# Optimization experiments

Measured on AMD Instinct MI355X. Metric: run time of the kernel, lower is better.

## Reference

```python
import jax, jax.numpy as jnp
import numpy as np
from jax.ops import segment_sum, segment_max

N = 20000      # nodes
DEG = 16       # incoming edges per node
E = N * DEG    # edges
IN = 128       # in_features
BOND = 16      # bond_features_dim
OUT = 128      # output_features
NUM_LAYERS = 3
LEAKY = 0.2
ELU_ALPHA = 1.0


def _lin_params(key, out_f, in_f):
    kw, kb = jax.random.split(key)
    s = 1.0 / np.sqrt(in_f)
    w = jax.random.uniform(kw, (out_f, in_f), jnp.float32, -s, s)
    b = jax.random.uniform(kb, (out_f,), jnp.float32, -s, s)
    return w, b


def setup_inputs() -> dict:
    key = jax.random.key(0)
    ks = jax.random.split(key, 20)
    atom_features = jax.random.normal(ks[0], (N, IN), jnp.float32)
    edge_src = jax.random.randint(ks[1], (E,), 0, N, jnp.int32)
    # every node receives exactly DEG edges (avoids the isolated-node bug path)
    edge_dst = jnp.repeat(jnp.arange(N, dtype=jnp.int32), DEG)
    bond_features = jax.random.normal(ks[2], (E, BOND), jnp.float32)

    v1_fc1_w, v1_fc1_b = _lin_params(ks[3], OUT, IN)
    v1_fc2_w, v1_fc2_b = _lin_params(ks[4], OUT, IN + BOND)
    v1_att_w, v1_att_b = _lin_params(ks[5], 1, 2 * OUT)
    v1_attend_w, v1_attend_b = _lin_params(ks[6], OUT, OUT)
    v1_gru_wih, v1_gru_bih = _lin_params(ks[7], 3 * OUT, OUT)
    v1_gru_whh, v1_gru_bhh = _lin_params(ks[8], 3 * OUT, OUT)

    v2_fc1_w, v2_fc1_b = _lin_params(ks[9], 1, 2 * OUT)
    v2_fc2_w, v2_fc2_b = _lin_params(ks[10], OUT, OUT)
    v2_gru_wih, v2_gru_bih = _lin_params(ks[11], 3 * OUT, OUT)
    v2_gru_whh, v2_gru_bhh = _lin_params(ks[12], 3 * OUT, OUT)

    lin_w, lin_b = _lin_params(ks[13], OUT, OUT)

    return dict(atom_features=atom_features, edge_src=edge_src, edge_dst=edge_dst,
                bond_features=bond_features,
                v1_fc1_w=v1_fc1_w, v1_fc1_b=v1_fc1_b, v1_fc2_w=v1_fc2_w, v1_fc2_b=v1_fc2_b,
                v1_att_w=v1_att_w, v1_att_b=v1_att_b, v1_attend_w=v1_attend_w, v1_attend_b=v1_attend_b,
                v1_gru_wih=v1_gru_wih, v1_gru_whh=v1_gru_whh, v1_gru_bih=v1_gru_bih, v1_gru_bhh=v1_gru_bhh,
                v2_fc1_w=v2_fc1_w, v2_fc1_b=v2_fc1_b, v2_fc2_w=v2_fc2_w, v2_fc2_b=v2_fc2_b,
                v2_gru_wih=v2_gru_wih, v2_gru_whh=v2_gru_whh, v2_gru_bih=v2_gru_bih, v2_gru_bhh=v2_gru_bhh,
                lin_w=lin_w, lin_b=lin_b)


def _linear(x, w, b):
    return x @ w.T + b


def _gru_cell(x, h, wih, whh, bih, bhh):
    gi = x @ wih.T + bih   # [N, 3*OUT]
    gh = h @ whh.T + bhh
    i_r, i_z, i_n = jnp.split(gi, 3, axis=-1)
    h_r, h_z, h_n = jnp.split(gh, 3, axis=-1)
    r = jax.nn.sigmoid(i_r + h_r)
    z = jax.nn.sigmoid(i_z + h_z)
    n = jnp.tanh(i_n + r * h_n)
    return (1.0 - z) * n + z * h


def _segment_softmax(logits, seg, n):
    m = segment_max(logits, seg, num_segments=n)
    ex = jnp.exp(logits - m[seg])
    den = segment_sum(ex, seg, num_segments=n)
    return ex / den[seg]


def reference(atom_features, edge_src, edge_dst, bond_features,
              v1_fc1_w, v1_fc1_b, v1_fc2_w, v1_fc2_b, v1_att_w, v1_att_b,
              v1_attend_w, v1_attend_b, v1_gru_wih, v1_gru_whh, v1_gru_bih, v1_gru_bhh,
              v2_fc1_w, v2_fc1_b, v2_fc2_w, v2_fc2_b,
              v2_gru_wih, v2_gru_whh, v2_gru_bih, v2_gru_bhh,
              lin_w, lin_b):
    n = atom_features.shape[0]
    lrelu = lambda x: jax.nn.leaky_relu(x, negative_slope=LEAKY)

    # ---- GATlayerV1 ----
    new_atom = lrelu(_linear(atom_features, v1_fc1_w, v1_fc1_b))           # [N, OUT]
    nbr_trans = _linear(new_atom, v1_attend_w, v1_attend_b)                # [N, OUT]
    nbr_in = jnp.concatenate([atom_features[edge_src], bond_features], axis=1)  # [E, IN+BOND]
    nbr = lrelu(_linear(nbr_in, v1_fc2_w, v1_fc2_b))                       # [E, OUT]
    pair = jnp.concatenate([new_atom[edge_dst], nbr], axis=1)              # [E, 2*OUT]
    logits = lrelu(_linear(pair, v1_att_w, v1_att_b))[:, 0]                # [E]
    score = _segment_softmax(logits, edge_dst, n)                          # [E]
    transform = segment_sum(score[:, None] * nbr_trans[edge_src], edge_dst, num_segments=n)
    ctx = jax.nn.elu(transform, alpha=ELU_ALPHA)
    h = _gru_cell(ctx, new_atom, v1_gru_wih, v1_gru_whh, v1_gru_bih, v1_gru_bhh)
    G_0 = new_atom

    all_tensors = [h]

    # ---- GATlayerV2 (shared weights across layers 2..NUM_LAYERS) ----
    for _ in range(NUM_LAYERS - 1):
        nt = _linear(h, v2_fc2_w, v2_fc2_b)                                # [N, OUT]
        pair2 = jnp.concatenate([h[edge_dst], h[edge_src]], axis=1)        # [E, 2*OUT]
        lg = lrelu(_linear(pair2, v2_fc1_w, v2_fc1_b))[:, 0]               # [E]
        sc = _segment_softmax(lg, edge_dst, n)
        tr = segment_sum(sc[:, None] * nt[edge_src], edge_dst, num_segments=n)
        ctx2 = jax.nn.elu(tr, alpha=ELU_ALPHA)
        h = _gru_cell(ctx2, h, v2_gru_wih, v2_gru_whh, v2_gru_bih, v2_gru_bhh)
        all_tensors.append(h)

    all_stack = jnp.stack(all_tensors)           # [NUM_LAYERS, N, OUT]
    averaged = all_stack.mean(axis=0)            # [N, OUT]
    output = jax.nn.gelu(_linear(averaged, lin_w, lin_b), approximate=False)
    return (output, all_stack, G_0, averaged)
```

## Files before the change

kernel.cpp:

```cpp
#include <hip/hip_runtime.h>
#include <math.h>

#define NN 20000
#define EE 320000

using short8 = __attribute__((ext_vector_type(8))) short;
using f32x4  = __attribute__((ext_vector_type(4))) float;
using f32x2  = __attribute__((ext_vector_type(2))) float;
using u16x4  = __attribute__((ext_vector_type(4))) unsigned short;

__device__ __forceinline__ unsigned short f2bf(float x) {
    union { float f; unsigned u; } v; v.f = x;
    unsigned r = (v.u + 0x7fffu + ((v.u >> 16) & 1u)) >> 16;
    return (unsigned short)r;
}
__device__ __forceinline__ float bf2f(unsigned short b) {
    union { unsigned u; float f; } v; v.u = ((unsigned)b) << 16;
    return v.f;
}
__device__ __forceinline__ float sigmoidf_(float x) { return 1.f / (1.f + __expf(-x)); }
__device__ __forceinline__ float tanhf_(float x) {
    float e = __expf(-2.f * x);
    return (1.f - e) / (1.f + e);
}
__device__ __forceinline__ float lrelu_(float x) { return x > 0.f ? x : 0.2f * x; }
__device__ __forceinline__ float elu_(float x) { return x > 0.f ? x : __expf(x) - 1.f; }

__device__ __forceinline__ unsigned pk_fp8x4(float a, float b, float c, float d) {
    int w = 0;
    w = __builtin_amdgcn_cvt_pk_fp8_f32(a, b, w, false);
    w = __builtin_amdgcn_cvt_pk_fp8_f32(c, d, w, true);
    return (unsigned)w;
}
__device__ __forceinline__ void up_fp8x4(unsigned w, float* o) {
    f32x2 lo = __builtin_amdgcn_cvt_pk_f32_fp8((int)w, false);
    f32x2 hi = __builtin_amdgcn_cvt_pk_f32_fp8((int)w, true);
    o[0] = lo[0]; o[1] = lo[1]; o[2] = hi[0]; o[3] = hi[1];
}

struct PackDesc { const float* w; unsigned short* out; int O; int ldw; int mode; };
struct PackArgs { PackDesc d[10]; };

__global__ void k_pack(PackArgs args) {
    PackDesc d = args.d[blockIdx.y];
    int idx = blockIdx.x * 256 + threadIdx.x;
    if (d.mode == 1) {
        if (idx >= 512) return;
        int t = idx >> 6, l = idx & 63;
        int lr = l & 15, lg = l >> 4;
        int ch = lr * 8 + t;
        short8 o;
        #pragma unroll
        for (int j = 0; j < 8; j++) {
            int k = lg * 8 + j;
            o[j] = (k < 16) ? (short)f2bf(d.w[(size_t)ch * 144 + 128 + k]) : (short)0;
        }
        *(short8*)(d.out + (size_t)idx * 8) = o;
        return;
    }
    int total = (d.O / 16) * 4 * 64;
    if (idx >= total) return;
    int l = idx & 63, rest = idx >> 6;
    int ko = rest & 3, no = rest >> 2;
    int row = no * 16 + (l & 15);
    int col0 = ko * 32 + ((l >> 4) * 8);
    const float* src = d.w + (size_t)row * d.ldw + col0;
    unsigned short o[8];
    #pragma unroll
    for (int j = 0; j < 8; j++) o[j] = f2bf(src[j]);
    #pragma unroll
    for (int j = 0; j < 8; j++) d.out[(size_t)idx * 8 + j] = o[j];
}

__global__ __launch_bounds__(256) void k_v1_front(
    const float* __restrict__ atom,
    const unsigned short* __restrict__ Bfc1, const unsigned short* __restrict__ BW2a,
    const float* __restrict__ fc1_b, const float* __restrict__ fc2_b,
    const float* __restrict__ attw,
    float* __restrict__ g0, unsigned short* __restrict__ naBf,
    unsigned char* __restrict__ naF8,
    unsigned char* __restrict__ U8, float* __restrict__ adst)
{
    __shared__ float Xs[16][132];
    __shared__ unsigned short Ys2[16 * 128];
    const int tid = threadIdx.x, l = tid & 63, w = tid >> 6;
    const int lr = l & 15, lg = l >> 4;
    const int m0 = blockIdx.x * 16;

    f32x4 acc1[2] = {}, accU[2] = {};
    #pragma unroll
    for (int ko = 0; ko < 4; ko++) {
        const f32x4* ap = (const f32x4*)(atom + (size_t)(m0 + lr) * 128 + ko * 32 + lg * 8);
        f32x4 a0 = __builtin_nontemporal_load(ap);
        f32x4 a1 = __builtin_nontemporal_load(ap + 1);
        short8 af;
        #pragma unroll
        for (int j = 0; j < 4; j++) { af[j] = (short)f2bf(a0[j]); af[4 + j] = (short)f2bf(a1[j]); }
        #pragma unroll
        for (int i = 0; i < 2; i++) {
            int t = w * 2 + i;
            short8 b1 = *(const short8*)(Bfc1 + ((size_t)(t * 4 + ko) * 64 + l) * 8);
            acc1[i] = __builtin_amdgcn_mfma_f32_16x16x32_bf16(af, b1, acc1[i], 0, 0, 0);
            short8 bu = *(const short8*)(BW2a + ((size_t)(t * 4 + ko) * 64 + l) * 8);
            accU[i] = __builtin_amdgcn_mfma_f32_16x16x32_bf16(af, bu, accU[i], 0, 0, 0);
        }
    }
    #pragma unroll
    for (int i = 0; i < 2; i++) {
        int col = (w * 2 + i) * 16 + lr;
        float b1v = fc1_b[col], bUv = fc2_b[col];
        #pragma unroll
        for (int r = 0; r < 4; r++) {
            int row = lg * 4 + r;
            float v = lrelu_(acc1[i][r] + b1v);
            Xs[row][col] = v;
            Ys2[row * 128 + col] = f2bf(accU[i][r] + bUv);
        }
    }
    __syncthreads();
    {
        short8 uy = *(const short8*)(Ys2 + tid * 8);
        float uf[8];
        #pragma unroll
        for (int j = 0; j < 8; j++) uf[j] = bf2f((unsigned short)uy[j]);
        uint2 o8;
        o8.x = pk_fp8x4(uf[0], uf[1], uf[2], uf[3]);
        o8.y = pk_fp8x4(uf[4], uf[5], uf[6], uf[7]);
        *(uint2*)(U8 + (size_t)m0 * 128 + tid * 8) = o8;
    }
    {
        int row = tid >> 4, q = tid & 15;
        short8 tmp;
        float p = 0.f;
        float vv[8];
        #pragma unroll
        for (int j = 0; j < 8; j++) {
            float x = Xs[row][q * 8 + j];
            vv[j] = x;
            tmp[j] = (short)f2bf(x);
            p = fmaf(x, attw[q * 8 + j], p);
        }
        __builtin_nontemporal_store(*(f32x4*)vv,
            (f32x4*)(g0 + (size_t)(m0 + row) * 128 + q * 8));
        __builtin_nontemporal_store(*(f32x4*)(vv + 4),
            (f32x4*)(g0 + (size_t)(m0 + row) * 128 + q * 8 + 4));
        *(short8*)(naBf + (size_t)(m0 + row) * 128 + q * 8) = tmp;
        uint2 n8;
        n8.x = pk_fp8x4(vv[0], vv[1], vv[2], vv[3]);
        n8.y = pk_fp8x4(vv[4], vv[5], vv[6], vv[7]);
        *(uint2*)(naF8 + (size_t)(m0 + row) * 128 + q * 8) = n8;
        #pragma unroll
        for (int m = 1; m <= 8; m <<= 1) p += __shfl_xor(p, m, 16);
        if (q == 0) adst[m0 + row] = p;
    }
}

template<int AGGMODE, int FRONT, int FINAL>
__global__ __launch_bounds__(512, 4) void k_gru(
    const float* __restrict__ aD, const float* __restrict__ bS, const float* __restrict__ b1,
    const float* __restrict__ bond, const unsigned short* __restrict__ BW2b,
    const float* __restrict__ attw, const float* __restrict__ attb1,
    const float* __restrict__ adst, const unsigned char* __restrict__ U8,
    const int* __restrict__ esrc, const unsigned char* __restrict__ V8,
    const unsigned short* __restrict__ Bpre, const float* __restrict__ bpre,
    const unsigned short* __restrict__ Bih, const unsigned short* __restrict__ Bhh,
    const float* __restrict__ bih, const float* __restrict__ bhh,
    const unsigned short* __restrict__ hprevBf, float* __restrict__ houtF,
    unsigned short* __restrict__ houtBf, unsigned char* __restrict__ houtF8,
    const float* __restrict__ w2att, float* __restrict__ aDOut, float* __restrict__ bSOut,
    const float* __restrict__ as0, const float* __restrict__ as1,
    const unsigned short* __restrict__ Blin, const float* __restrict__ linb,
    float* __restrict__ avgOut, float* __restrict__ outF)
{
    __shared__ unsigned short aggS[16][136];
    __shared__ unsigned short ctxS[16][136];
    __shared__ unsigned short hpS[16][136];
    __shared__ float lgS[(AGGMODE == 0) ? 16 : 1][16];
    const int tid = threadIdx.x, l = tid & 63, w = tid >> 6;
    const int lr = l & 15, lg = l >> 4;
    const int m0 = blockIdx.x * 16;
    const int r2 = tid >> 5, c4 = (tid & 31) * 4;

    *(u16x4*)&hpS[r2][c4] = *(const u16x4*)(hprevBf + (size_t)(m0 + r2) * 128 + c4);

    if (AGGMODE == 0) {
        float aw[8];
        #pragma unroll
        for (int t = 0; t < 8; t++) aw[t] = attw[128 + lr * 8 + t];
        const float ab = attb1[0];
        #pragma unroll
        for (int nn = 0; nn < 2; nn++) {
            const int n = m0 + w * 2 + nn;
            const int e0 = n * 16;
            short8 af = {};
            if (lg < 2) {
                const f32x4* bp = (const f32x4*)(bond + (size_t)(e0 + lr) * 16 + lg * 8);
                f32x4 b0 = __builtin_nontemporal_load(bp);
                f32x4 b1v = __builtin_nontemporal_load(bp + 1);
                #pragma unroll
                for (int j = 0; j < 4; j++) {
                    af[j] = (short)f2bf(b0[j]); af[4 + j] = (short)f2bf(b1v[j]);
                }
            }
            f32x4 c[8];
            #pragma unroll
            for (int t = 0; t < 8; t++) {
                short8 bw = *(const short8*)(BW2b + (size_t)(t * 64 + l) * 8);
                f32x4 z = {};
                c[t] = __builtin_amdgcn_mfma_f32_16x16x32_bf16(af, bw, z, 0, 0, 0);
            }
            float s[4];
            #pragma unroll
            for (int r = 0; r < 4; r++) {
                int e = e0 + lg * 4 + r;
                int src = esrc[e];
                uint2 u2 = *(const uint2*)(U8 + (size_t)src * 128 + lr * 8);
                float uf[8];
                up_fp8x4(u2.x, uf);
                up_fp8x4(u2.y, uf + 4);
                float a0 = 0.f;
                #pragma unroll
                for (int t = 0; t < 8; t++)
                    a0 = fmaf(aw[t], lrelu_(c[t][r] + uf[t]), a0);
                s[r] = a0;
            }
            #pragma unroll
            for (int mk = 1; mk <= 8; mk <<= 1)
                #pragma unroll
                for (int r = 0; r < 4; r++) s[r] += __shfl_xor(s[r], mk, 16);
            if (lr == 0) {
                float anode = adst[n];
                #pragma unroll
                for (int r = 0; r < 4; r++)
                    lgS[w * 2 + nn][lg * 4 + r] = lrelu_(anode + ab + s[r]);
            }
        }
    }
    __syncthreads();

    const int g2 = tid >> 5;
    const int q2 = tid & 31;
    const int q = q2 & 15;
    const int hf = q2 >> 4;
    float wq;
    int srcq;
    {
        const int gnode = m0 + g2;
        const int e = gnode * 16 + q;
        srcq = esrc[e];
        float lgt;
        if (AGGMODE == 0) lgt = lgS[g2][q];
        else              lgt = lrelu_(aD[gnode] + bS[srcq] + b1[0]);
        float mx = lgt;
        #pragma unroll
        for (int mk = 1; mk <= 8; mk <<= 1) mx = fmaxf(mx, __shfl_xor(mx, mk, 16));
        float ex = __expf(lgt - mx);
        float den = ex;
        #pragma unroll
        for (int mk = 1; mk <= 8; mk <<= 1) den += __shfl_xor(den, mk, 16);
        wq = ex / den;
    }

    unsigned gv[16];
    #pragma unroll
    for (int i = 0; i < 16; i++) {
        int si = __shfl(srcq, i, 16);
        gv[i] = *(const unsigned*)(V8 + (size_t)si * 128 + hf * 64 + q * 4);
    }

    f32x4 ah[3] = {};
    #pragma unroll
    for (int ko = 0; ko < 4; ko++) {
        short8 afh = *(const short8*)&hpS[lr][ko * 32 + lg * 8];
        #pragma unroll
        for (int g = 0; g < 3; g++) {
            short8 bh = *(const short8*)(Bhh + ((size_t)((w + 8 * g) * 4 + ko) * 64 + l) * 8);
            ah[g] = __builtin_amdgcn_mfma_f32_16x16x32_bf16(afh, bh, ah[g], 0, 0, 0);
        }
    }

    {
        float s[4] = {};
        #pragma unroll
        for (int i = 0; i < 16; i++) {
            float wi = __shfl(wq, i, 16);
            float d[4];
            up_fp8x4(gv[i], d);
            #pragma unroll
            for (int j = 0; j < 4; j++) s[j] = fmaf(wi, d[j], s[j]);
        }
        u16x4 o;
        #pragma unroll
        for (int j = 0; j < 4; j++) o[j] = f2bf(s[j]);
        *(u16x4*)&aggS[g2][hf * 64 + q * 4] = o;
    }
    __syncthreads();

    f32x4 accp = {};
    #pragma unroll
    for (int ko = 0; ko < 4; ko++) {
        short8 afA = *(const short8*)&aggS[lr][ko * 32 + lg * 8];
        short8 bfp = *(const short8*)(Bpre + ((size_t)(w * 4 + ko) * 64 + l) * 8);
        accp = __builtin_amdgcn_mfma_f32_16x16x32_bf16(afA, bfp, accp, 0, 0, 0);
    }
    {
        const int col = w * 16 + lr;
        const float bb = bpre[col];
        #pragma unroll
        for (int r = 0; r < 4; r++)
            ctxS[lg * 4 + r][col] = f2bf(elu_(accp[r] + bb));
    }
    __syncthreads();

    f32x4 ai[3] = {};
    #pragma unroll
    for (int ko = 0; ko < 4; ko++) {
        short8 afc = *(const short8*)&ctxS[lr][ko * 32 + lg * 8];
        #pragma unroll
        for (int g = 0; g < 3; g++) {
            short8 bi = *(const short8*)(Bih + ((size_t)((w + 8 * g) * 4 + ko) * 64 + l) * 8);
            ai[g] = __builtin_amdgcn_mfma_f32_16x16x32_bf16(afc, bi, ai[g], 0, 0, 0);
        }
    }
    {
        const int c = w * 16 + lr;
        const float br = bih[c] + bhh[c];
        const float bz = bih[c + 128] + bhh[c + 128];
        const float bin_ = bih[c + 256];
        const float bhn = bhh[c + 256];
        #pragma unroll
        for (int r = 0; r < 4; r++) {
            const int lrow = lg * 4 + r;
            float rg = sigmoidf_(ai[0][r] + ah[0][r] + br);
            float zg = sigmoidf_(ai[1][r] + ah[1][r] + bz);
            float ng = tanhf_(ai[2][r] + bin_ + rg * (ah[2][r] + bhn));
            float hp = bf2f(hpS[lrow][c]);
            hpS[lrow][c] = f2bf(fmaf(zg, hp - ng, ng));
        }
    }
    __syncthreads();

    {
        u16x4 hv = *(const u16x4*)&hpS[r2][c4];
        f32x4 vf;
        #pragma unroll
        for (int j = 0; j < 4; j++) vf[j] = bf2f(hv[j]);
        __builtin_nontemporal_store(vf, (f32x4*)(houtF + (size_t)(m0 + r2) * 128 + c4));
        if (FINAL == 0) {
            *(u16x4*)(houtBf + (size_t)(m0 + r2) * 128 + c4) = hv;
            *(unsigned*)(houtF8 + (size_t)(m0 + r2) * 128 + c4) =
                pk_fp8x4(vf[0], vf[1], vf[2], vf[3]);
        }
    }

    if (FRONT) {
        if (tid < 256) {
            int row = tid >> 4, qq = tid & 15;
            short8 hv8 = *(const short8*)&hpS[row][qq * 8];
            float pa = 0.f, pb = 0.f;
            #pragma unroll
            for (int j = 0; j < 8; j++) {
                float x = bf2f((unsigned short)hv8[j]);
                pa = fmaf(x, w2att[qq * 8 + j], pa);
                pb = fmaf(x, w2att[128 + qq * 8 + j], pb);
            }
            #pragma unroll
            for (int m = 1; m <= 8; m <<= 1) {
                pa += __shfl_xor(pa, m, 16);
                pb += __shfl_xor(pb, m, 16);
            }
            if (qq == 0) { aDOut[m0 + row] = pa; bSOut[m0 + row] = pb; }
        }
    }

    if (FINAL) {
        {
            f32x4 x0 = __builtin_nontemporal_load(
                (const f32x4*)(as0 + (size_t)(m0 + r2) * 128 + c4));
            f32x4 x1 = __builtin_nontemporal_load(
                (const f32x4*)(as1 + (size_t)(m0 + r2) * 128 + c4));
            u16x4 hv = *(const u16x4*)&hpS[r2][c4];
            f32x4 av;
            #pragma unroll
            for (int j = 0; j < 4; j++)
                av[j] = (x0[j] + x1[j] + bf2f(hv[j])) * (1.f / 3.f);
            __builtin_nontemporal_store(av, (f32x4*)(avgOut + (size_t)(m0 + r2) * 128 + c4));
            u16x4 ab16;
            #pragma unroll
            for (int j = 0; j < 4; j++) ab16[j] = f2bf(av[j]);
            *(u16x4*)&ctxS[r2][c4] = ab16;
        }
        __syncthreads();
        f32x4 acc2 = {};
        #pragma unroll
        for (int ko = 0; ko < 4; ko++) {
            short8 af = *(const short8*)&ctxS[lr][ko * 32 + lg * 8];
            short8 bf = *(const short8*)(Blin + ((size_t)(w * 4 + ko) * 64 + l) * 8);
            acc2 = __builtin_amdgcn_mfma_f32_16x16x32_bf16(af, bf, acc2, 0, 0, 0);
        }
        {
            const int col = w * 16 + lr;
            const float bb = linb[col];
            #pragma unroll
            for (int r = 0; r < 4; r++) {
                float vv = acc2[r] + bb;
                vv = 0.5f * vv * (1.f + erff(vv * 0.70710678118654752f));
                aggS[lg * 4 + r][col] = f2bf(vv);
            }
        }
        __syncthreads();
        {
            u16x4 ov = *(const u16x4*)&aggS[r2][c4];
            f32x4 vf;
            #pragma unroll
            for (int j = 0; j < 4; j++) vf[j] = bf2f(ov[j]);
            __builtin_nontemporal_store(vf, (f32x4*)(outF + (size_t)(m0 + r2) * 128 + c4));
        }
    }
}

extern "C" void kernel_launch(void* const* d_in, const int* in_sizes, int n_in,
                              void* d_out, int out_size, void* d_ws, size_t ws_size,
                              hipStream_t stream) {
    const float* atom     = (const float*)d_in[0];
    const int*   esrc     = (const int*)d_in[1];
    const float* bond     = (const float*)d_in[3];
    const float* fc1_w    = (const float*)d_in[4];
    const float* fc1_b    = (const float*)d_in[5];
    const float* fc2_w    = (const float*)d_in[6];
    const float* fc2_b    = (const float*)d_in[7];
    const float* att_w    = (const float*)d_in[8];
    const float* att_b    = (const float*)d_in[9];
    const float* attend_w = (const float*)d_in[10];
    const float* attend_b = (const float*)d_in[11];
    const float* gih1     = (const float*)d_in[12];
    const float* ghh1     = (const float*)d_in[13];
    const float* bih1     = (const float*)d_in[14];
    const float* bhh1     = (const float*)d_in[15];
    const float* fc1v2_w  = (const float*)d_in[16];
    const float* fc1v2_b  = (const float*)d_in[17];
    const float* fc2v2_w  = (const float*)d_in[18];
    const float* fc2v2_b  = (const float*)d_in[19];
    const float* gih2     = (const float*)d_in[20];
    const float* ghh2     = (const float*)d_in[21];
    const float* bih2     = (const float*)d_in[22];
    const float* bhh2     = (const float*)d_in[23];
    const float* lin_w    = (const float*)d_in[24];
    const float* lin_b    = (const float*)d_in[25];

    char* wsb = (char*)d_ws;
    size_t off = 0;
    auto allocB = [&](size_t bytes) {
        size_t o = off; off = (off + bytes + 255) & ~(size_t)255; return o;
    };
    unsigned short* Bfc1   = (unsigned short*)(wsb + allocB(128 * 128 * 2));
    unsigned short* Batt   = (unsigned short*)(wsb + allocB(128 * 128 * 2));
    unsigned short* BW2a   = (unsigned short*)(wsb + allocB(128 * 128 * 2));
    unsigned short* BW2b   = (unsigned short*)(wsb + allocB(512 * 8 * 2));
    unsigned short* Bgih1  = (unsigned short*)(wsb + allocB(384 * 128 * 2));
    unsigned short* Bghh1  = (unsigned short*)(wsb + allocB(384 * 128 * 2));
    unsigned short* Bfc2v2 = (unsigned short*)(wsb + allocB(128 * 128 * 2));
    unsigned short* Bgih2  = (unsigned short*)(wsb + allocB(384 * 128 * 2));
    unsigned short* Bghh2  = (unsigned short*)(wsb + allocB(384 * 128 * 2));
    unsigned short* Blin   = (unsigned short*)(wsb + allocB(128 * 128 * 2));
    unsigned short* naBf   = (unsigned short*)(wsb + allocB((size_t)NN * 128 * 2));
    unsigned short* h1Bf   = (unsigned short*)(wsb + allocB((size_t)NN * 128 * 2));
    unsigned short* h2Bf   = (unsigned short*)(wsb + allocB((size_t)NN * 128 * 2));
    unsigned char*  U8     = (unsigned char*)(wsb + allocB((size_t)NN * 128));
    unsigned char*  naF8   = (unsigned char*)(wsb + allocB((size_t)NN * 128));
    unsigned char*  h1F8   = (unsigned char*)(wsb + allocB((size_t)NN * 128));
    unsigned char*  h2F8   = (unsigned char*)(wsb + allocB((size_t)NN * 128));
    float* adst   = (float*)(wsb + allocB((size_t)NN * 4));
    float* aD     = (float*)(wsb + allocB((size_t)NN * 4));
    float* bS     = (float*)(wsb + allocB((size_t)NN * 4));
    (void)ws_size;

    float* out0 = (float*)d_out;
    float* as0  = out0 + (size_t)NN * 128;
    float* as1  = as0 + (size_t)NN * 128;
    float* as2  = as1 + (size_t)NN * 128;
    float* g0   = out0 + (size_t)4 * NN * 128;
    float* avg  = out0 + (size_t)5 * NN * 128;

    PackArgs pa;
    pa.d[0] = { fc1_w,    Bfc1,   128, 128, 0 };
    pa.d[1] = { attend_w, Batt,   128, 128, 0 };
    pa.d[2] = { fc2_w,    BW2a,   128, 144, 0 };
    pa.d[3] = { gih1,     Bgih1,  384, 128, 0 };
    pa.d[4] = { ghh1,     Bghh1,  384, 128, 0 };
    pa.d[5] = { fc2v2_w,  Bfc2v2, 128, 128, 0 };
    pa.d[6] = { gih2,     Bgih2,  384, 128, 0 };
    pa.d[7] = { ghh2,     Bghh2,  384, 128, 0 };
    pa.d[8] = { lin_w,    Blin,   128, 128, 0 };
    pa.d[9] = { fc2_w,    BW2b,   0,   0,   1 };
    k_pack<<<dim3(24, 10), 256, 0, stream>>>(pa);

    const int GB = NN / 16;

    k_v1_front<<<GB, 256, 0, stream>>>(atom, Bfc1, BW2a, fc1_b, fc2_b, att_w,
                                       g0, naBf, naF8, U8, adst);
    k_gru<0, 1, 0><<<GB, 512, 0, stream>>>(
        nullptr, nullptr, nullptr,
        bond, BW2b, att_w, att_b, adst, U8,
        esrc, naF8,
        Batt, attend_b,
        Bgih1, Bghh1, bih1, bhh1, naBf, as0, h1Bf, h1F8,
        fc1v2_w, aD, bS,
        nullptr, nullptr, nullptr, nullptr, nullptr, nullptr);

    k_gru<1, 1, 0><<<GB, 512, 0, stream>>>(
        aD, bS, fc1v2_b,
        nullptr, nullptr, nullptr, nullptr, nullptr, nullptr,
        esrc, h1F8,
        Bfc2v2, fc2v2_b,
        Bgih2, Bghh2, bih2, bhh2, h1Bf, as1, h2Bf, h2F8,
        fc1v2_w, aD, bS,
        nullptr, nullptr, nullptr, nullptr, nullptr, nullptr);

    k_gru<1, 0, 1><<<GB, 512, 0, stream>>>(
        aD, bS, fc1v2_b,
        nullptr, nullptr, nullptr, nullptr, nullptr, nullptr,
        esrc, h2F8,
        Bfc2v2, fc2v2_b,
        Bgih2, Bghh2, bih2, bhh2, h2Bf, as2, nullptr, nullptr,
        nullptr, nullptr, nullptr,
        as0, as1, Blin, lin_b, avg, out0);
}
```

Measured before the change: 113.6 us.

## Halve k_gru block to 256 threads, two column tiles per wave

Shrinks the fused GRU/attention kernel from 512 to 256 threads per 16-node block, so each of the 4 waves now computes two 16-column MFMA tiles per gate and each thread handles 8 features in the gather and store phases. Work per thread doubles, which raises register pressure but cuts the number of waves taking part in each barrier and amortizes A-fragment LDS loads across two B tiles. With fewer waves per block, latency hiding relies on more concurrent blocks per CU, and occupancy could drop if registers grow.

```diff
diff --git a/kernel.cpp b/kernel.cpp
--- a/kernel.cpp
+++ b/kernel.cpp
@@ -156,7 +156,7 @@
 }
 
 template<int AGGMODE, int FRONT, int FINAL>
-__global__ __launch_bounds__(512, 4) void k_gru(
+__global__ __launch_bounds__(256, 4) void k_gru(
     const float* __restrict__ aD, const float* __restrict__ bS, const float* __restrict__ b1,
     const float* __restrict__ bond, const unsigned short* __restrict__ BW2b,
     const float* __restrict__ attw, const float* __restrict__ attb1,
@@ -179,9 +179,9 @@
     const int tid = threadIdx.x, l = tid & 63, w = tid >> 6;
     const int lr = l & 15, lg = l >> 4;
     const int m0 = blockIdx.x * 16;
-    const int r2 = tid >> 5, c4 = (tid & 31) * 4;
-
-    *(u16x4*)&hpS[r2][c4] = *(const u16x4*)(hprevBf + (size_t)(m0 + r2) * 128 + c4);
+    const int r2 = tid >> 4, sc0 = (tid & 15) * 8;
+
+    *(short8*)&hpS[r2][sc0] = *(const short8*)(hprevBf + (size_t)(m0 + r2) * 128 + sc0);
 
     if (AGGMODE == 0) {
         float aw[8];
@@ -189,8 +189,8 @@
         for (int t = 0; t < 8; t++) aw[t] = attw[128 + lr * 8 + t];
         const float ab = attb1[0];
         #pragma unroll
-        for (int nn = 0; nn < 2; nn++) {
-            const int n = m0 + w * 2 + nn;
+        for (int nn = 0; nn < 4; nn++) {
+            const int n = m0 + w * 4 + nn;
             const int e0 = n * 16;
             short8 af = {};
             if (lg < 2) {
@@ -232,22 +232,19 @@
                 float anode = adst[n];
                 #pragma unroll
                 for (int r = 0; r < 4; r++)
-                    lgS[w * 2 + nn][lg * 4 + r] = lrelu_(anode + ab + s[r]);
+                    lgS[w * 4 + nn][lg * 4 + r] = lrelu_(anode + ab + s[r]);
             }
         }
     }
     __syncthreads();
 
-    const int g2 = tid >> 5;
-    const int q2 = tid & 31;
-    const int q = q2 & 15;
-    const int hf = q2 >> 4;
+    const int g2 = tid >> 4;
+    const int q = tid & 15;
     float wq;
     int srcq;
     {
         const int gnode = m0 + g2;
-        const int e = gnode * 16 + q;
-        srcq = esrc[e];
+        srcq = esrc[gnode * 16 + q];
         float lgt;
         if (AGGMODE == 0) lgt = lgS[g2][q];
         else              lgt = lrelu_(aD[gnode] + bS[srcq] + b1[0]);
@@ -261,69 +258,81 @@
         wq = ex / den;
     }
 
-    unsigned gv[16];
+    uint2 gv[16];
     #pragma unroll
     for (int i = 0; i < 16; i++) {
         int si = __shfl(srcq, i, 16);
-        gv[i] = *(const unsigned*)(V8 + (size_t)si * 128 + hf * 64 + q * 4);
-    }
-
-    f32x4 ah[3] = {};
+        gv[i] = *(const uint2*)(V8 + (size_t)si * 128 + q * 8);
+    }
+
+    f32x4 ah[2][3] = {};
     #pragma unroll
     for (int ko = 0; ko < 4; ko++) {
         short8 afh = *(const short8*)&hpS[lr][ko * 32 + lg * 8];
         #pragma unroll
-        for (int g = 0; g < 3; g++) {
-            short8 bh = *(const short8*)(Bhh + ((size_t)((w + 8 * g) * 4 + ko) * 64 + l) * 8);
-            ah[g] = __builtin_amdgcn_mfma_f32_16x16x32_bf16(afh, bh, ah[g], 0, 0, 0);
-        }
+        for (int g = 0; g < 3; g++)
+            #pragma unroll
+            for (int ct = 0; ct < 2; ct++) {
+                int t = w + ct * 4 + 8 * g;
+                short8 bh = *(const short8*)(Bhh + ((size_t)(t * 4 + ko) * 64 + l) * 8);
+                ah[ct][g] = __builtin_amdgcn_mfma_f32_16x16x32_bf16(afh, bh, ah[ct][g], 0, 0, 0);
+            }
     }
 
     {
-        float s[4] = {};
+        float s[8] = {};
         #pragma unroll
         for (int i = 0; i < 16; i++) {
             float wi = __shfl(wq, i, 16);
-            float d[4];
-            up_fp8x4(gv[i], d);
-            #pragma unroll
-            for (int j = 0; j < 4; j++) s[j] = fmaf(wi, d[j], s[j]);
-        }
-        u16x4 o;
-        #pragma unroll
-        for (int j = 0; j < 4; j++) o[j] = f2bf(s[j]);
-        *(u16x4*)&aggS[g2][hf * 64 + q * 4] = o;
+            float d[8];
+            up_fp8x4(gv[i].x, d);
+            up_fp8x4(gv[i].y, d + 4);
+            #pragma unroll
+            for (int j = 0; j < 8; j++) s[j] = fmaf(wi, d[j], s[j]);
+        }
+        short8 o;
+        #pragma unroll
+        for (int j = 0; j < 8; j++) o[j] = (short)f2bf(s[j]);
+        *(short8*)&aggS[g2][q * 8] = o;
     }
     __syncthreads();
 
-    f32x4 accp = {};
+    f32x4 accp[2] = {};
     #pragma unroll
     for (int ko = 0; ko < 4; ko++) {
         short8 afA = *(const short8*)&aggS[lr][ko * 32 + lg * 8];
-        short8 bfp = *(const short8*)(Bpre + ((size_t)(w * 4 + ko) * 64 + l) * 8);
-        accp = __builtin_amdgcn_mfma_f32_16x16x32_bf16(afA, bfp, accp, 0, 0, 0);
-    }
-    {
-        const int col = w * 16 + lr;
+        #pragma unroll
+        for (int ct = 0; ct < 2; ct++) {
+            short8 bfp = *(const short8*)(Bpre + ((size_t)((w + ct * 4) * 4 + ko) * 64 + l) * 8);
+            accp[ct] = __builtin_amdgcn_mfma_f32_16x16x32_bf16(afA, bfp, accp[ct], 0, 0, 0);
+        }
+    }
+    #pragma unroll
+    for (int ct = 0; ct < 2; ct++) {
+        const int col = (w + ct * 4) * 16 + lr;
         const float bb = bpre[col];
         #pragma unroll
         for (int r = 0; r < 4; r++)
-            ctxS[lg * 4 + r][col] = f2bf(elu_(accp[r] + bb));
+            ctxS[lg * 4 + r][col] = f2bf(elu_(accp[ct][r] + bb));
     }
     __syncthreads();
 
-    f32x4 ai[3] = {};
+    f32x4 ai[2][3] = {};
     #pragma unroll
     for (int ko = 0; ko < 4; ko++) {
         short8 afc = *(const short8*)&ctxS[lr][ko * 32 + lg * 8];
         #pragma unroll
-        for (int g = 0; g < 3; g++) {
-            short8 bi = *(const short8*)(Bih + ((size_t)((w + 8 * g) * 4 + ko) * 64 + l) * 8);
-            ai[g] = __builtin_amdgcn_mfma_f32_16x16x32_bf16(afc, bi, ai[g], 0, 0, 0);
-        }
-    }
-    {
-        const int c = w * 16 + lr;
+        for (int g = 0; g < 3; g++)
+            #pragma unroll
+            for (int ct = 0; ct < 2; ct++) {
+                int t = w + ct * 4 + 8 * g;
+                short8 bi = *(const short8*)(Bih + ((size_t)(t * 4 + ko) * 64 + l) * 8);
+                ai[ct][g] = __builtin_amdgcn_mfma_f32_16x16x32_bf16(afc, bi, ai[ct][g], 0, 0, 0);
+            }
+    }
+    #pragma unroll
+    for (int ct = 0; ct < 2; ct++) {
+        const int c = (w + ct * 4) * 16 + lr;
         const float br = bih[c] + bhh[c];
         const float bz = bih[c + 128] + bhh[c + 128];
         const float bin_ = bih[c + 256];
@@ -331,9 +340,9 @@
         #pragma unroll
         for (int r = 0; r < 4; r++) {
             const int lrow = lg * 4 + r;
-            float rg = sigmoidf_(ai[0][r] + ah[0][r] + br);
-            float zg = sigmoidf_(ai[1][r] + ah[1][r] + bz);
-            float ng = tanhf_(ai[2][r] + bin_ + rg * (ah[2][r] + bhn));
+            float rg = sigmoidf_(ai[ct][0][r] + ah[ct][0][r] + br);
+            float zg = sigmoidf_(ai[ct][1][r] + ah[ct][1][r] + bz);
+            float ng = tanhf_(ai[ct][2][r] + bin_ + rg * (ah[ct][2][r] + bhn));
             float hp = bf2f(hpS[lrow][c]);
             hpS[lrow][c] = f2bf(fmaf(zg, hp - ng, ng));
         }
@@ -341,80 +350,91 @@
     __syncthreads();
 
     {
-        u16x4 hv = *(const u16x4*)&hpS[r2][c4];
-        f32x4 vf;
-        #pragma unroll
-        for (int j = 0; j < 4; j++) vf[j] = bf2f(hv[j]);
-        __builtin_nontemporal_store(vf, (f32x4*)(houtF + (size_t)(m0 + r2) * 128 + c4));
+        short8 hv = *(const short8*)&hpS[r2][sc0];
+        float vf[8];
+        #pragma unroll
+        for (int j = 0; j < 8; j++) vf[j] = bf2f((unsigned short)hv[j]);
+        f32x4* dst = (f32x4*)(houtF + (size_t)(m0 + r2) * 128 + sc0);
+        __builtin_nontemporal_store(*(f32x4*)vf, dst);
+        __builtin_nontemporal_store(*(f32x4*)(vf + 4), dst + 1);
         if (FINAL == 0) {
-            *(u16x4*)(houtBf + (size_t)(m0 + r2) * 128 + c4) = hv;
-            *(unsigned*)(houtF8 + (size_t)(m0 + r2) * 128 + c4) =
-                pk_fp8x4(vf[0], vf[1], vf[2], vf[3]);
+            *(short8*)(houtBf + (size_t)(m0 + r2) * 128 + sc0) = hv;
+            uint2 h8;
+            h8.x = pk_fp8x4(vf[0], vf[1], vf[2], vf[3]);
+            h8.y = pk_fp8x4(vf[4], vf[5], vf[6], vf[7]);
+            *(uint2*)(houtF8 + (size_t)(m0 + r2) * 128 + sc0) = h8;
         }
     }
 
     if (FRONT) {
-        if (tid < 256) {
-            int row = tid >> 4, qq = tid & 15;
-            short8 hv8 = *(const short8*)&hpS[row][qq * 8];
-            float pa = 0.f, pb = 0.f;
-            #pragma unroll
-            for (int j = 0; j < 8; j++) {
-                float x = bf2f((unsigned short)hv8[j]);
-                pa = fmaf(x, w2att[qq * 8 + j], pa);
-                pb = fmaf(x, w2att[128 + qq * 8 + j], pb);
-            }
-            #pragma unroll
-            for (int m = 1; m <= 8; m <<= 1) {
-                pa += __shfl_xor(pa, m, 16);
-                pb += __shfl_xor(pb, m, 16);
-            }
-            if (qq == 0) { aDOut[m0 + row] = pa; bSOut[m0 + row] = pb; }
-        }
+        int row = tid >> 4, qq = tid & 15;
+        float pa = 0.f, pb = 0.f;
+        #pragma unroll
+        for (int j = 0; j < 8; j++) {
+            float x = bf2f(hpS[row][qq * 8 + j]);
+            pa = fmaf(x, w2att[qq * 8 + j], pa);
+            pb = fmaf(x, w2att[128 + qq * 8 + j], pb);
+        }
+        #pragma unroll
+        for (int m = 1; m <= 8; m <<= 1) {
+            pa += __shfl_xor(pa, m, 16);
+            pb += __shfl_xor(pb, m, 16);
+        }
+        if (qq == 0) { aDOut[m0 + row] = pa; bSOut[m0 + row] = pb; }
     }
 
     if (FINAL) {
         {
-            f32x4 x0 = __builtin_nontemporal_load(
-                (const f32x4*)(as0 + (size_t)(m0 + r2) * 128 + c4));
-            f32x4 x1 = __builtin_nontemporal_load(
-                (const f32x4*)(as1 + (size_t)(m0 + r2) * 128 + c4));
-            u16x4 hv = *(const u16x4*)&hpS[r2][c4];
-            f32x4 av;
-            #pragma unroll
-            for (int j = 0; j < 4; j++)
-                av[j] = (x0[j] + x1[j] + bf2f(hv[j])) * (1.f / 3.f);
-            __builtin_nontemporal_store(av, (f32x4*)(avgOut + (size_t)(m0 + r2) * 128 + c4));
-            u16x4 ab16;
-            #pragma unroll
-            for (int j = 0; j < 4; j++) ab16[j] = f2bf(av[j]);
-            *(u16x4*)&ctxS[r2][c4] = ab16;
+            const f32x4* p0 = (const f32x4*)(as0 + (size_t)(m0 + r2) * 128 + sc0);
+            const f32x4* p1 = (const f32x4*)(as1 + (size_t)(m0 + r2) * 128 + sc0);
+            f32x4* pav = (f32x4*)(avgOut + (size_t)(m0 + r2) * 128 + sc0);
+            short8 hv = *(const short8*)&hpS[r2][sc0];
+            short8 ab16;
+            #pragma unroll
+            for (int k = 0; k < 2; k++) {
+                f32x4 x0 = __builtin_nontemporal_load(p0 + k);
+                f32x4 x1 = __builtin_nontemporal_load(p1 + k);
+                f32x4 av;
+                #pragma unroll
+                for (int j = 0; j < 4; j++) {
+                    av[j] = (x0[j] + x1[j] + bf2f((unsigned short)hv[k * 4 + j])) * (1.f / 3.f);
+                    ab16[k * 4 + j] = (short)f2bf(av[j]);
+                }
+                __builtin_nontemporal_store(av, pav + k);
+            }
+            *(short8*)&ctxS[r2][sc0] = ab16;
         }
         __syncthreads();
-        f32x4 acc2 = {};
+        f32x4 acc2[2] = {};
         #pragma unroll
         for (int ko = 0; ko < 4; ko++) {
             short8 af = *(const short8*)&ctxS[lr][ko * 32 + lg * 8];
-            short8 bf = *(const short8*)(Blin + ((size_t)(w * 4 + ko) * 64 + l) * 8);
-            acc2 = __builtin_amdgcn_mfma_f32_16x16x32_bf16(af, bf, acc2, 0, 0, 0);
-        }
-        {
-            const int col = w * 16 + lr;
+            #pragma unroll
+            for (int ct = 0; ct < 2; ct++) {
+                short8 bf = *(const short8*)(Blin + ((size_t)((w + ct * 4) * 4 + ko) * 64 + l) * 8);
+                acc2[ct] = __builtin_amdgcn_mfma_f32_16x16x32_bf16(af, bf, acc2[ct], 0, 0, 0);
+            }
+        }
+        #pragma unroll
+        for (int ct = 0; ct < 2; ct++) {
+            const int col = (w + ct * 4) * 16 + lr;
             const float bb = linb[col];
             #pragma unroll
             for (int r = 0; r < 4; r++) {
-                float vv = acc2[r] + bb;
+                float vv = acc2[ct][r] + bb;
                 vv = 0.5f * vv * (1.f + erff(vv * 0.70710678118654752f));
                 aggS[lg * 4 + r][col] = f2bf(vv);
             }
         }
         __syncthreads();
         {
-            u16x4 ov = *(const u16x4*)&aggS[r2][c4];
-            f32x4 vf;
-            #pragma unroll
-            for (int j = 0; j < 4; j++) vf[j] = bf2f(ov[j]);
-            __builtin_nontemporal_store(vf, (f32x4*)(outF + (size_t)(m0 + r2) * 128 + c4));
+            short8 ov = *(const short8*)&aggS[r2][sc0];
+            float vf[8];
+            #pragma unroll
+            for (int j = 0; j < 8; j++) vf[j] = bf2f((unsigned short)ov[j]);
+            f32x4* dst = (f32x4*)(outF + (size_t)(m0 + r2) * 128 + sc0);
+            __builtin_nontemporal_store(*(f32x4*)vf, dst);
+            __builtin_nontemporal_store(*(f32x4*)(vf + 4), dst + 1);
         }
     }
 }
@@ -499,7 +519,7 @@
 
     k_v1_front<<<GB, 256, 0, stream>>>(atom, Bfc1, BW2a, fc1_b, fc2_b, att_w,
                                        g0, naBf, naF8, U8, adst);
-    k_gru<0, 1, 0><<<GB, 512, 0, stream>>>(
+    k_gru<0, 1, 0><<<GB, 256, 0, stream>>>(
         nullptr, nullptr, nullptr,
         bond, BW2b, att_w, att_b, adst, U8,
         esrc, naF8,
@@ -508,7 +528,7 @@
         fc1v2_w, aD, bS,
         nullptr, nullptr, nullptr, nullptr, nullptr, nullptr);
 
-    k_gru<1, 1, 0><<<GB, 512, 0, stream>>>(
+    k_gru<1, 1, 0><<<GB, 256, 0, stream>>>(
         aD, bS, fc1v2_b,
         nullptr, nullptr, nullptr, nullptr, nullptr, nullptr,
         esrc, h1F8,
@@ -517,7 +537,7 @@
         fc1v2_w, aD, bS,
         nullptr, nullptr, nullptr, nullptr, nullptr, nullptr);
 
-    k_gru<1, 0, 1><<<GB, 512, 0, stream>>>(
+    k_gru<1, 0, 1><<<GB, 256, 0, stream>>>(
         aD, bS, fc1v2_b,
         nullptr, nullptr, nullptr, nullptr, nullptr, nullptr,
         esrc, h2F8,
```

After: 118.9 us. 1.05x slower.
